# Kernel optimization log

Measured on AMD Instinct MI355X. Metric: run time of the kernel, lower is better.

The kernel has to match this reference:

```python
import jax, jax.numpy as jnp
import numpy as np

D = 192
HEADS = 4
HD = D // HEADS
R = 3  # correlation radius actually used in forward_level
NDISP = (2 * R + 1) ** 2  # 49
T = 3  # frames -> 2 consecutive pairs
ITERS = 4


def layer_norm(x, w, b, eps=1e-5):
    m = jnp.mean(x, axis=-1, keepdims=True)
    v = jnp.var(x, axis=-1, keepdims=True)
    return (x - m) / jnp.sqrt(v + eps) * w + b


def mha(x, in_w, in_b, out_w, out_b):
    # torch nn.MultiheadAttention, batch_first, self-attention
    B, N, _ = x.shape
    qkv = x @ in_w.T + in_b
    q, k, v = jnp.split(qkv, 3, axis=-1)
    q = q.reshape(B, N, HEADS, HD).transpose(0, 2, 1, 3) * (1.0 / float(np.sqrt(HD)))
    k = k.reshape(B, N, HEADS, HD).transpose(0, 2, 1, 3)
    v = v.reshape(B, N, HEADS, HD).transpose(0, 2, 1, 3)
    att = jax.nn.softmax(jnp.einsum('bhqd,bhkd->bhqk', q, k), axis=-1)
    y = jnp.einsum('bhqk,bhkd->bhqd', att, v).transpose(0, 2, 1, 3).reshape(B, N, D)
    return y @ out_w.T + out_b


def tblock(x, p):
    ln1w, ln1b, inw, inb, ow, ob, ln2w, ln2b, w1, b1, w2, b2 = p
    x = x + mha(layer_norm(x, ln1w, ln1b), inw, inb, ow, ob)
    h = layer_norm(x, ln2w, ln2b)
    h = jax.nn.gelu(h @ w1.T + b1, approximate=False) @ w2.T + b2
    return x + h


def local_corr(f1, f2):
    C = f1.shape[1]
    scale = 1.0 / float(np.sqrt(C))
    outs = []
    for dy in range(-R, R + 1):
        for dx in range(-R, R + 1):
            f2s = jnp.roll(f2, (dy, dx), axis=(2, 3))
            outs.append(jnp.sum(f1 * f2s, axis=1) * scale)
    return jnp.stack(outs, axis=1)


def grid_sample_bilinear_border(img, grid):
    # img: B,C,H,W; grid: B,Ho,Wo,2 with (x,y) in [-1,1]; align_corners=True, border padding
    B, C, H, W = img.shape
    x = jnp.clip((grid[..., 0] + 1.0) * 0.5 * (W - 1), 0.0, W - 1)
    y = jnp.clip((grid[..., 1] + 1.0) * 0.5 * (H - 1), 0.0, H - 1)
    x0 = jnp.floor(x); y0 = jnp.floor(y)
    x1 = jnp.minimum(x0 + 1, W - 1); y1 = jnp.minimum(y0 + 1, H - 1)
    wx = (x - x0)[:, None]; wy = (y - y0)[:, None]
    imgf = img.reshape(B, C, H * W)
    Ho, Wo = x.shape[1], x.shape[2]
    def gather(yy, xx):
        idx = (yy * W + xx).astype(jnp.int32).reshape(B, 1, Ho * Wo)
        return jnp.take_along_axis(imgf, idx, axis=2).reshape(B, C, Ho, Wo)
    v00 = gather(y0, x0); v01 = gather(y0, x1)
    v10 = gather(y1, x0); v11 = gather(y1, x1)
    return v00 * (1 - wx) * (1 - wy) + v01 * wx * (1 - wy) + v10 * (1 - wx) * wy + v11 * wx * wy


def warp(img, flow):
    # flow in pixels, Bx2xHxW
    B, C, H, W = img.shape
    xs = jnp.linspace(-1.0, 1.0, W); ys = jnp.linspace(-1.0, 1.0, H)
    gx, gy = jnp.meshgrid(xs, ys)  # each (H, W), 'xy' indexing
    base = jnp.stack([gx, gy], axis=-1)[None]
    off = jnp.stack([flow[:, 0] * (2.0 / max(W - 1, 1)),
                     flow[:, 1] * (2.0 / max(H - 1, 1))], axis=-1)
    return grid_sample_bilinear_border(img, base + off)


def upsample2x_align(img):
    # F.interpolate(scale_factor=2, mode='bilinear', align_corners=True)
    B, C, H, W = img.shape
    Ho, Wo = 2 * H, 2 * W
    xs = jnp.linspace(-1.0, 1.0, Wo); ys = jnp.linspace(-1.0, 1.0, Ho)
    gx, gy = jnp.meshgrid(xs, ys)
    grid = jnp.broadcast_to(jnp.stack([gx, gy], axis=-1)[None], (B, Ho, Wo, 2))
    return grid_sample_bilinear_border(img, grid)


def conv2d(x, w, b):
    y = jax.lax.conv_general_dilated(x, w, (1, 1), ((1, 1), (1, 1)),
                                     dimension_numbers=('NCHW', 'OIHW', 'NCHW'))
    return y + b[None, :, None, None]


def _forward(feats_l1, feats_l2, feats_l3, tok_w, tok_b,
             lcm_ln1_w, lcm_ln1_b, lcm_in_w, lcm_in_b, lcm_out_w, lcm_out_b,
             lcm_ln2_w, lcm_ln2_b, lcm_mlp_w1, lcm_mlp_b1, lcm_mlp_w2, lcm_mlp_b2,
             gtr_ln1_w, gtr_ln1_b, gtr_in_w, gtr_in_b, gtr_out_w, gtr_out_b,
             gtr_ln2_w, gtr_ln2_b, gtr_mlp_w1, gtr_mlp_b1, gtr_mlp_w2, gtr_mlp_b2,
             head_w1, head_b1, head_w2, head_b2,
             ref1_w1, ref1_b1, ref1_w2, ref1_b2,
             ref0_w1, ref0_b1, ref0_w2, ref0_b2):
    feats = [[feats_l1[t] for t in range(T)],
             [feats_l2[t] for t in range(T)],
             [feats_l3[t] for t in range(T)]]
    # ---- CostTokenizer ----
    tokens = []
    for lvl in range(3):
        toks = []
        for k in range(T - 1):
            corr = local_corr(feats[lvl][k], feats[lvl][k + 1])
            toks.append(jnp.einsum('bchw,dc->bdhw', corr, tok_w[lvl]) + tok_b[lvl][None, :, None, None])
        tokens.append(toks)
    lcm_p = [(lcm_ln1_w[i], lcm_ln1_b[i], lcm_in_w[i], lcm_in_b[i], lcm_out_w[i], lcm_out_b[i],
              lcm_ln2_w[i], lcm_ln2_b[i], lcm_mlp_w1[i], lcm_mlp_b1[i], lcm_mlp_w2[i], lcm_mlp_b2[i])
             for i in range(lcm_ln1_w.shape[0])]
    gtr_p = [(gtr_ln1_w[i], gtr_ln1_b[i], gtr_in_w[i], gtr_in_b[i], gtr_out_w[i], gtr_out_b[i],
              gtr_ln2_w[i], gtr_ln2_b[i], gtr_mlp_w1[i], gtr_mlp_b1[i], gtr_mlp_w2[i], gtr_mlp_b2[i])
             for i in range(gtr_ln1_w.shape[0])]
    # ---- LatentCostMemory (EMA state; .detach() -> stop_gradient; state resets when N changes) ----
    state = None
    latent = []
    for toks in tokens:
        lvl_lat = []
        for tok in toks:
            B_, Dd, H, W = tok.shape
            x = tok.reshape(B_, Dd, H * W).transpose(0, 2, 1)  # b (h w) d
            for p in lcm_p:
                x = tblock(x, p)
            if state is None or state.shape[1] != x.shape[1]:
                state = jax.lax.stop_gradient(x)
            x = 0.8 * x + 0.2 * state
            state = jax.lax.stop_gradient(x)
            lvl_lat.append(x.transpose(0, 2, 1))  # b d n
        latent.append(lvl_lat)
    H8, W8 = feats[1][0].shape[-2:]
    coarse = []
    for lat in latent[1]:
        x = lat.transpose(0, 2, 1)
        for p in gtr_p:
            x = tblock(x, p)
        fv = jax.nn.gelu(x @ head_w1.T + head_b1, approximate=False) @ head_w2.T + head_b2
        coarse.append(fv.transpose(0, 2, 1).reshape(-1, 2, H8, W8))
    # ---- MSRecurrentDecoder ----
    outs = []
    for k, f8 in enumerate(coarse):
        cur = f8
        for _ in range(ITERS):
            w10 = warp(feats[1][k + 1], cur)
            x = jnp.concatenate([feats[1][k], cur, w10], axis=1)
            cur = cur + conv2d(jax.nn.gelu(conv2d(x, ref1_w1, ref1_b1), approximate=False), ref1_w2, ref1_b2)
        cur2 = upsample2x_align(cur)
        for _ in range(ITERS):
            w10 = warp(feats[0][k + 1], cur2)
            x = jnp.concatenate([feats[0][k], cur2, w10], axis=1)
            cur2 = cur2 + conv2d(jax.nn.gelu(conv2d(x, ref0_w1, ref0_b1), approximate=False), ref0_w2, ref0_b2)
        outs.append(cur2)
    return jnp.stack(outs)  # [pairs, B, 2, H/4, W/4]


def setup_inputs():
    key = jax.random.key(0)
    ks = iter(jax.random.split(key, 64))
    def rn(shape, s=1.0):
        return jax.random.normal(next(ks), shape, dtype=jnp.float32) * s
    B = 1
    inp = {}
    inp['feats_l1'] = rn((T, B, 64, 64, 64))
    inp['feats_l2'] = rn((T, B, 128, 32, 32))
    inp['feats_l3'] = rn((T, B, 192, 16, 16))
    inp['tok_w'] = rn((3, D, NDISP), 0.02)
    inp['tok_b'] = rn((3, D), 0.02)
    for pre, n in (('lcm', 6), ('gtr', 2)):
        inp[pre + '_ln1_w'] = jnp.ones((n, D), jnp.float32)
        inp[pre + '_ln1_b'] = jnp.zeros((n, D), jnp.float32)
        inp[pre + '_in_w'] = rn((n, 3 * D, D), 0.02)
        inp[pre + '_in_b'] = rn((n, 3 * D), 0.02)
        inp[pre + '_out_w'] = rn((n, D, D), 0.02)
        inp[pre + '_out_b'] = rn((n, D), 0.02)
        inp[pre + '_ln2_w'] = jnp.ones((n, D), jnp.float32)
        inp[pre + '_ln2_b'] = jnp.zeros((n, D), jnp.float32)
        inp[pre + '_mlp_w1'] = rn((n, 4 * D, D), 0.02)
        inp[pre + '_mlp_b1'] = rn((n, 4 * D), 0.02)
        inp[pre + '_mlp_w2'] = rn((n, D, 4 * D), 0.02)
        inp[pre + '_mlp_b2'] = rn((n, D), 0.02)
    inp['head_w1'] = rn((D, D), 0.02); inp['head_b1'] = rn((D,), 0.02)
    inp['head_w2'] = rn((2, D), 0.02); inp['head_b2'] = rn((2,), 0.02)
    inp['ref1_w1'] = rn((128, 258, 3, 3), 0.02); inp['ref1_b1'] = rn((128,), 0.02)
    inp['ref1_w2'] = rn((2, 128, 3, 3), 0.02); inp['ref1_b2'] = rn((2,), 0.02)
    inp['ref0_w1'] = rn((64, 130, 3, 3), 0.02); inp['ref0_b1'] = rn((64,), 0.02)
    inp['ref0_w2'] = rn((2, 64, 3, 3), 0.02); inp['ref0_b2'] = rn((2,), 0.02)
    return inp


def reference(feats_l1, feats_l2, feats_l3, tok_w, tok_b,
              lcm_ln1_w, lcm_ln1_b, lcm_in_w, lcm_in_b, lcm_out_w, lcm_out_b,
              lcm_ln2_w, lcm_ln2_b, lcm_mlp_w1, lcm_mlp_b1, lcm_mlp_w2, lcm_mlp_b2,
              gtr_ln1_w, gtr_ln1_b, gtr_in_w, gtr_in_b, gtr_out_w, gtr_out_b,
              gtr_ln2_w, gtr_ln2_b, gtr_mlp_w1, gtr_mlp_b1, gtr_mlp_w2, gtr_mlp_b2,
              head_w1, head_b1, head_w2, head_b2,
              ref1_w1, ref1_b1, ref1_w2, ref1_b2,
              ref0_w1, ref0_b1, ref0_w2, ref0_b2):
    return _forward(feats_l1, feats_l2, feats_l3, tok_w, tok_b,
                    lcm_ln1_w, lcm_ln1_b, lcm_in_w, lcm_in_b, lcm_out_w, lcm_out_b,
                    lcm_ln2_w, lcm_ln2_b, lcm_mlp_w1, lcm_mlp_b1, lcm_mlp_w2, lcm_mlp_b2,
                    gtr_ln1_w, gtr_ln1_b, gtr_in_w, gtr_in_b, gtr_out_w, gtr_out_b,
                    gtr_ln2_w, gtr_ln2_b, gtr_mlp_w1, gtr_mlp_b1, gtr_mlp_w2, gtr_mlp_b2,
                    head_w1, head_b1, head_w2, head_b2,
                    ref1_w1, ref1_b1, ref1_w2, ref1_b2,
                    ref0_w1, ref0_b1, ref0_w2, ref0_b2)
```

## Files before the change

kernel.cpp:

```cpp
#include <hip/hip_runtime.h>
#include <hip/hip_bf16.h>

typedef __hip_bfloat16 bf16;
typedef short bf16x8 __attribute__((ext_vector_type(8)));
typedef float f32x4 __attribute__((ext_vector_type(4)));

#define DEV __device__ __forceinline__

DEV float bf2f(bf16 v) { return __bfloat162float(v); }
DEV bf16 f2bf(float v) { return __float2bfloat16(v); }
DEV unsigned short bfr(float f) {
  bf16 h = __float2bfloat16(f);
  return *reinterpret_cast<unsigned short*>(&h);
}
DEV float shf(unsigned short u) {
  unsigned int x = ((unsigned int)u) << 16;
  return *reinterpret_cast<float*>(&x);
}
DEV float gelu_exact(float x) { return 0.5f * x * (1.0f + erff(x * 0.70710678118654752f)); }

DEV float ldw(const void* p, long i, int isb) {
  return isb ? __bfloat162float(((const bf16*)p)[i]) : ((const float*)p)[i];
}

__global__ void k_detect(const unsigned short* __restrict__ u, int* __restrict__ flag) {
  __shared__ int bad;
  if (threadIdx.x == 0) bad = 0;
  __syncthreads();
  for (int i = threadIdx.x; i < 8192; i += 256) {
    int expo = (u[i] >> 7) & 0xFF;
    if (expo >= 138) atomicOr(&bad, 1);
  }
  __syncthreads();
  if (threadIdx.x == 0) *flag = bad ? 0 : 1;
}
__global__ void k_setone(int* p) { *p = 1; }

__global__ void k_cvt(const void* __restrict__ s, float* __restrict__ d, int n,
                      const int* __restrict__ fl) {
  int isb = *fl;
  int i = blockIdx.x * blockDim.x + threadIdx.x;
  if (i < n) d[i] = ldw(s, i, isb);
}

__global__ void k_zerosh(unsigned short* __restrict__ p, int n8) {
  int i = blockIdx.x * blockDim.x + threadIdx.x;
  if (i < n8) { uint4 z = {0, 0, 0, 0}; *(uint4*)(p + (long)i * 8) = z; }
}

__global__ void k_padtokw(const void* __restrict__ tw, bf16* __restrict__ dst,
                          const int* __restrict__ fl) {
  int isb = *fl;
  int i = blockIdx.x * blockDim.x + threadIdx.x;
  if (i >= 12288) return;
  int n = i >> 6, k = i & 63;
  float v = (k < 49) ? ldw(tw, 9408 + (long)n * 49 + k, isb) : 0.0f;
  dst[i] = f2bf(v);
}

__global__ void k_packw(const void* __restrict__ src, bf16* __restrict__ dst,
                        int OC, int C, int ICT, int NP, int ICP, int n,
                        const int* __restrict__ fl) {
  int isb = *fl;
  int i = blockIdx.x * blockDim.x + threadIdx.x;
  if (i >= n) return;
  int s = i / (NP * ICP);
  int r = i - s * NP * ICP;
  int oc = r / ICP, icp = r - oc * ICP;
  float v = 0.0f;
  if (oc < OC) {
    int ic = -1;
    if (icp < C) ic = icp;
    else if (icp < 2 * C) ic = icp - C + C + 2;
    else if (icp < 2 * C + 2) ic = icp - 2 * C + C;
    if (ic >= 0 && ic < ICT) v = ldw(src, ((long)oc * ICT + ic) * 9 + s, isb);
  }
  dst[i] = f2bf(v);
}

__global__ void k_trans_feats(const void* __restrict__ in, bf16* __restrict__ Fp,
                              int F, int C, int HW, const int* __restrict__ fl) {
  int isb = *fl;
  int cpg = C >> 3;
  int n = F * HW * cpg;
  int i = blockIdx.x * blockDim.x + threadIdx.x;
  if (i >= n) return;
  int p = i % HW;
  int rem = i / HW;
  int c8 = rem % cpg;
// ... 147 lines not shown
  for (int t = 0; t < 9; ++t) {
    int dy = t / 3, dx = t - dy * 3;
    const unsigned short* ar = base + ((long)dy * Wp2 + dx) * C;
    const unsigned short* w0r = wb + (long)(t * 16 + 0) * C;
    const unsigned short* w1r = wb + (long)(t * 16 + 1) * C;
    if (CPL == 2) {
      unsigned int a = *(const unsigned int*)ar;
      unsigned int q0 = *(const unsigned int*)w0r;
      unsigned int q1 = *(const unsigned int*)w1r;
      float a0 = shf((unsigned short)a), a1 = shf((unsigned short)(a >> 16));
      s0 += a0 * shf((unsigned short)q0) + a1 * shf((unsigned short)(q0 >> 16));
      s1 += a0 * shf((unsigned short)q1) + a1 * shf((unsigned short)(q1 >> 16));
    } else {
      float a0 = shf(ar[0]);
      s0 += a0 * shf(w0r[0]);
      s1 += a0 * shf(w1r[0]);
    }
  }
#pragma unroll
  for (int o = 32; o; o >>= 1) { s0 += __shfl_xor(s0, o); s1 += __shfl_xor(s1, o); }
  if (ln == 0) {
    cur[((long)b * 2 + 0) * HW + p] = s0 + b0 + r0;
    cur[((long)b * 2 + 1) * HW + p] = s1 + b1 + r1;
  }
}

__global__ void k_corr(const bf16* __restrict__ Fp2, bf16* __restrict__ corrT) {
  __shared__ unsigned short f1r[128];
  int p = blockIdx.x;
  int b = blockIdx.y;
  int t = threadIdx.x;
  const unsigned short* f1 = (const unsigned short*)Fp2 + ((long)b * 1024 + p) * 128;
  if (t < 16) *(uint4*)&f1r[t * 8] = *(const uint4*)(f1 + t * 8);
  __syncthreads();
  long rowo = ((long)b * 1024 + p) * 64;
  if (t < 49) {
    int dy = t / 7 - 3, dx = t % 7 - 3;
    int h = p >> 5, w = p & 31;
    int p2 = (((h - dy) & 31) << 5) | ((w - dx) & 31);
    const unsigned short* f2 = (const unsigned short*)Fp2 + ((long)(b + 1) * 1024 + p2) * 128;
    float s = 0.0f;
    for (int c = 0; c < 128; c += 8) {
      union { unsigned short u[8]; uint4 v; } av = { .v = *(const uint4*)&f1r[c] };
      union { unsigned short u[8]; uint4 v; } bv = { .v = *(const uint4*)(f2 + c) };
#pragma unroll
      for (int j = 0; j < 8; ++j) s += shf(av.u[j]) * shf(bv.u[j]);
    }
    corrT[rowo + t] = f2bf(s * 0.08838834764831845f);
  } else {
    corrT[rowo + t] = f2bf(0.0f);
  }
}

template <int KT, int NTW, int ACT, bool HASRES, int AMODE, int OUTBF, int VT>
__global__ __launch_bounds__(64, 2) void k_gemm_w(
    const void* __restrict__ A, const void* __restrict__ W, long woff,
    const void* __restrict__ bias, long boff, const int* __restrict__ flb,
    const float* __restrict__ res, void* __restrict__ C,
    int N, const int* __restrict__ fl,
    const unsigned short* __restrict__ mop, const float* __restrict__ mml,
    bf16* __restrict__ vtout,
    const void* __restrict__ lnw, long lnwoff,
    const void* __restrict__ lnb, long lnboff) {
  constexpr int NK = KT / 32;
  int isb = *fl;
  int ln = threadIdx.x;
  int quad = ln >> 4, l16 = ln & 15;
  int m0 = blockIdx.y * 16, n0 = blockIdx.x * (16 * NTW);
  __shared__ unsigned short Als[(AMODE >= 2) ? 16 : 1][200];
  if constexpr (AMODE == 3) {
    int row = ln >> 2, j = ln & 3;
    const float* xr = (const float*)A + (long)(m0 + row) * 192 + j * 48;
    float av[48];
#pragma unroll
    for (int q = 0; q < 12; ++q) {
      float4 v = *(const float4*)(xr + q * 4);
      av[q * 4 + 0] = v.x; av[q * 4 + 1] = v.y;
      av[q * 4 + 2] = v.z; av[q * 4 + 3] = v.w;
    }
    float sum = 0.0f;
#pragma unroll
    for (int q = 0; q < 48; ++q) sum += av[q];
    sum += __shfl_xor(sum, 1);
    sum += __shfl_xor(sum, 2);
    float mean = sum * (1.0f / 192.0f);
    float vs = 0.0f;
#pragma unroll
    for (int q = 0; q < 48; ++q) { float d = av[q] - mean; vs += d * d; }
    vs += __shfl_xor(vs, 1);
    vs += __shfl_xor(vs, 2);
    float rstd = rsqrtf(vs * (1.0f / 192.0f) + 1e-5f);
#pragma unroll
    for (int g = 0; g < 6; ++g) {
      union { unsigned short u[8]; uint4 v; } pk;
#pragma unroll
      for (int e = 0; e < 8; ++e) {
        long k = j * 48 + g * 8 + e;
        float gg = ldw(lnw, lnwoff + k, isb);
        float bb = ldw(lnb, lnboff + k, isb);
        pk.u[e] = bfr((av[g * 8 + e] - mean) * rstd * gg + bb);
      }
      *(uint4*)&Als[row][j * 48 + g * 8] = pk.v;
    }
  } else if constexpr (AMODE == 2) {
    int row = ln >> 2, j = ln & 3;
    int m = m0 + row;
    int rr = m & 1023, bb = m >> 10;
    long idx[4];
    float ms[4], ls[4];
    float Ms = -1e30f;
#pragma unroll
    for (int s = 0; s < 4; ++s) {
      idx[s] = (((long)s * 2 + bb) * 4 + j) * 1024 + rr;
      ms[s] = mml[idx[s] * 2];
      ls[s] = mml[idx[s] * 2 + 1];
      Ms = fmaxf(Ms, ms[s]);
    }
    float e4[4], L = 0.0f;
#pragma unroll
    for (int s = 0; s < 4; ++s) { e4[s] = __expf(ms[s] - Ms); L += ls[s] * e4[s]; }
    float invL = 1.0f / L;
#pragma unroll
    for (int g = 0; g < 6; ++g) {
      union { unsigned short u[8]; uint4 v; } pk;
#pragma unroll
      for (int e2 = 0; e2 < 8; ++e2) {
        float o = 0.0f;
#pragma unroll
        for (int s = 0; s < 4; ++s) o += shf(mop[idx[s] * 48 + g * 8 + e2]) * e4[s];
        pk.u[e2] = bfr(o * invL);
      }
      *(uint4*)&Als[row][j * 48 + g * 8] = pk.v;
    }
  }
  f32x4 acc[NTW] = {};
  auto lda = [&](int kc) -> bf16x8 {
    if constexpr (AMODE >= 2) {
      return *(const bf16x8*)&Als[l16][kc * 32 + quad * 8];
    } else if constexpr (AMODE == 1) {
      return *(const bf16x8*)((const unsigned short*)A + (long)(m0 + l16) * KT + kc * 32 + quad * 8);
    } else {
      const float* ap = (const float*)A + (long)(m0 + l16) * KT + kc * 32 + quad * 8;
      float4 a0 = *(const float4*)ap;
      float4 a1 = *(const float4*)(ap + 4);
      union { unsigned short u[8]; bf16x8 v; } pk;
      pk.u[0] = bfr(a0.x); pk.u[1] = bfr(a0.y); pk.u[2] = bfr(a0.z); pk.u[3] = bfr(a0.w);
      pk.u[4] = bfr(a1.x); pk.u[5] = bfr(a1.y); pk.u[6] = bfr(a1.z); pk.u[7] = bfr(a1.w);
      return pk.v;
    }
  };
  if (isb) {
    const unsigned short* wb = (const unsigned short*)W + woff + (long)l16 * KT + quad * 8;
    for (int kc = 0; kc < NK; ++kc) {
      bf16x8 af = lda(kc);
#pragma unroll
      for (int nt = 0; nt < NTW; ++nt) {
        bf16x8 wf = *(const bf16x8*)(wb + (long)(n0 + nt * 16) * KT + kc * 32);
        acc[nt] = __builtin_amdgcn_mfma_f32_16x16x32_bf16(af, wf, acc[nt], 0, 0, 0);
      }
    }
  } else {
    const float* wb = (const float*)W + woff + (long)l16 * KT + quad * 8;
    for (int kc = 0; kc < NK; ++kc) {
      bf16x8 af = lda(kc);
#pragma unroll
      for (int nt = 0; nt < NTW; ++nt) {
        const float* wp = wb + (long)(n0 + nt * 16) * KT + kc * 32;
        float4 w0 = *(const float4*)wp;
        float4 w1 = *(const float4*)(wp + 4);
        union { unsigned short u[8]; bf16x8 v; } pk;
        pk.u[0] = bfr(w0.x); pk.u[1] = bfr(w0.y); pk.u[2] = bfr(w0.z); pk.u[3] = bfr(w0.w);
        pk.u[4] = bfr(w1.x); pk.u[5] = bfr(w1.y); pk.u[6] = bfr(w1.z); pk.u[7] = bfr(w1.w);
        acc[nt] = __builtin_amdgcn_mfma_f32_16x16x32_bf16(af, pk.v, acc[nt], 0, 0, 0);
      }
    }
  }
  int isbb = *flb;
#pragma unroll
  for (int nt = 0; nt < NTW; ++nt) {
    int n = n0 + nt * 16 + l16;
    float bv = ldw(bias, boff + n, isbb);
#pragma unroll
    for (int r = 0; r < 4; ++r) {
      int m = m0 + quad * 4 + r;
      float v = acc[nt][r] + bv;
      if (HASRES) v += res[(long)m * N + n];
      if (ACT == 1) v = gelu_exact(v);
      if (OUTBF) ((bf16*)C)[(long)m * N + n] = f2bf(v);
      else ((float*)C)[(long)m * N + n] = v;
      if constexpr (VT) {
        if (n >= 384) {
          int hh = (n - 384) / 48, dd = (n - 384) % 48;
          int row = m & 1023, bb = m >> 10;
          vtout[((long)(bb * 4 + hh) * 48 + dd) * 1024 + row] = f2bf(v);
        }
      }
    }
  }
}

__global__ __launch_bounds__(256) void k_head2(const float* __restrict__ A,
                                               const void* __restrict__ W,
                                               const void* __restrict__ bias,
                                               float* __restrict__ C,
                                               const int* __restrict__ fl) {
  int isb = *fl;
  int wv = threadIdx.x >> 6, ln = threadIdx.x & 63;
  int gw = blockIdx.x * 4 + wv;
  int m = gw >> 1, n = gw & 1;
  const float* a = A + (long)m * 192;
  float s = 0.0f;
#pragma unroll
  for (int q = 0; q < 3; ++q) {
    int j = ln + q * 64;
    s += a[j] * ldw(W, (long)n * 192 + j, isb);
  }
  for (int o = 32; o; o >>= 1) s += __shfl_xor(s, o);
  if (ln == 0) {
    int b = m >> 10, p = m & 1023;
    C[((long)b * 2 + n) * 1024 + p] = s + ldw(bias, n, isb);
  }
}

__global__ __launch_bounds__(256) void k_attn_mfma(const bf16* __restrict__ qkv,
                                                   const bf16* __restrict__ vt,
                                                   unsigned short* __restrict__ opart,
                                                   float* __restrict__ ml) {
  __shared__ unsigned short Qs[64][72];
  __shared__ unsigned short Ks[64][72];
  __shared__ unsigned short Vs[48][72];
  __shared__ unsigned short Ps[64][72];
  int tid = threadIdx.x;
  int wv = tid >> 6, ln = tid & 63, quad = ln >> 4, l16 = ln & 15;
  int h = blockIdx.y, b = blockIdx.z;
  int qt = blockIdx.x >> 2, s = blockIdx.x & 3;
  int q0 = qt * 64;
  const unsigned short* qp = (const unsigned short*)qkv + (long)b * 1024 * 576;
  const unsigned short* vp = (const unsigned short*)vt + ((long)(b * 4 + h) * 48) * 1024;
  for (int i = tid; i < 384; i += 256) {
    int r = i / 6, c = i % 6;
    *(uint4*)&Qs[r][c * 8] = *(const uint4*)(qp + (long)(q0 + r) * 576 + h * 48 + c * 8);
  }
  for (int i = tid; i < 128; i += 256) {
    int r = i >> 1, c = 6 + (i & 1);
    uint4 z = {0, 0, 0, 0};
    *(uint4*)&Qs[r][c * 8] = z;
  }
  float m[4] = {-1e30f, -1e30f, -1e30f, -1e30f};
  float l[4] = {0.0f, 0.0f, 0.0f, 0.0f};
  f32x4 accO[3] = {};
  const float SC = 0.14433756729740643f;
  for (int kc = s * 4; kc < s * 4 + 4; ++kc) {
    int k0 = kc * 64;
    for (int i = tid; i < 384; i += 256) {
      int r = i / 6, c = i % 6;
      *(uint4*)&Ks[r][c * 8] = *(const uint4*)(qp + (long)(k0 + r) * 576 + 192 + h * 48 + c * 8);
    }
    for (int i = tid; i < 128; i += 256) {
      int r = i >> 1, c = 6 + (i & 1);
      uint4 z = {0, 0, 0, 0};
      *(uint4*)&Ks[r][c * 8] = z;
    }
    for (int i = tid; i < 384; i += 256) {
      int d = i >> 3, c = i & 7;
      *(uint4*)&Vs[d][c * 8] = *(const uint4*)(vp + (long)d * 1024 + k0 + c * 8);
    }
    __syncthreads();
    f32x4 accS[4] = {};
    bf16x8 a0 = *(const bf16x8*)&Qs[wv * 16 + l16][quad * 8];
    bf16x8 a1 = *(const bf16x8*)&Qs[wv * 16 + l16][32 + quad * 8];
#pragma unroll
    for (int ct = 0; ct < 4; ++ct) {
      bf16x8 b0 = *(const bf16x8*)&Ks[ct * 16 + l16][quad * 8];
      bf16x8 b1 = *(const bf16x8*)&Ks[ct * 16 + l16][32 + quad * 8];
// ... 72 lines not shown
  int i = blockIdx.x * blockDim.x + threadIdx.x;
  if (i < 16384) {
    if (isb) ((bf16*)out)[i] = f2bf(cur2[i]);
    else ((float*)out)[i] = cur2[i];
  }
}

extern "C" void kernel_launch(void* const* d_in, const int* in_sizes, int n_in,
                              void* d_out, int out_size, void* d_ws, size_t ws_size,
                              hipStream_t stream) {
  const void* feats_l1 = d_in[0];
  const void* feats_l2 = d_in[1];
  const void* tok_w = d_in[3];
  const void* tok_b = d_in[4];
  const void* lcm_ln1_w = d_in[5];
  const void* lcm_ln1_b = d_in[6];
  const void* lcm_in_w  = d_in[7];
  const void* lcm_in_b  = d_in[8];
  const void* lcm_out_w = d_in[9];
  const void* lcm_out_b = d_in[10];
  const void* lcm_ln2_w = d_in[11];
  const void* lcm_ln2_b = d_in[12];
  const void* lcm_mlp_w1 = d_in[13];
  const void* lcm_mlp_b1 = d_in[14];
  const void* lcm_mlp_w2 = d_in[15];
  const void* lcm_mlp_b2 = d_in[16];
  const void* gtr_ln1_w = d_in[17];
  const void* gtr_ln1_b = d_in[18];
  const void* gtr_in_w  = d_in[19];
  const void* gtr_in_b  = d_in[20];
  const void* gtr_out_w = d_in[21];
  const void* gtr_out_b = d_in[22];
  const void* gtr_ln2_w = d_in[23];
  const void* gtr_ln2_b = d_in[24];
  const void* gtr_mlp_w1 = d_in[25];
  const void* gtr_mlp_b1 = d_in[26];
  const void* gtr_mlp_w2 = d_in[27];
  const void* gtr_mlp_b2 = d_in[28];
  const void* head_w1 = d_in[29];
  const void* head_b1 = d_in[30];
  const void* head_w2 = d_in[31];
  const void* head_b2 = d_in[32];
  const void* ref1_w1 = d_in[33];
  const void* ref1_b1 = d_in[34];
  const void* ref1_w2 = d_in[35];
  const void* ref1_b2 = d_in[36];
  const void* ref0_w1 = d_in[37];
  const void* ref0_b1 = d_in[38];
  const void* ref0_w2 = d_in[39];
  const void* ref0_b2 = d_in[40];
  (void)ws_size; (void)n_in; (void)in_sizes; (void)out_size;

  int* flag = (int*)d_ws;
  int* oneflag = (int*)d_ws + 2;
  float* wsf = (float*)d_ws;
  float* F2   = wsf + 16;
  float* rA   = F2 + 393216;
  float* rX   = rA + 786432;
  float* rT   = rX + 393216;
  float* rY   = rT + 393216;
  float* big  = rY + 393216;
  float* fv   = big + 1572864;
  float* cur  = fv + 4096;
  float* cur2 = cur + 4096;
  float* cb1a = cur2 + 16384;
  float* cb1b = cb1a + 128;
  float* cb0a = cb1b + 16;
  float* cb0b = cb0a + 64;
  bf16* wtok  = (bf16*)(cb0b + 16);
  float* wpk  = cb0b + 16 + 6144;
  bf16* w1p1 = (bf16*)wpk;
  bf16* w1p2 = (bf16*)(wpk + 165888);
  bf16* w0p1 = (bf16*)(wpk + 175104);
  bf16* w0p2 = (bf16*)(wpk + 221184);

  float* x = rX;
  bf16* corrTb = (bf16*)big;
  bf16* qkvbb  = (bf16*)big;
  bf16* vtb    = (bf16*)(big + 655360);
  bf16* hidb   = (bf16*)big;
  unsigned short* opart = (unsigned short*)rA;
  float* mlbuf = rY;
  float* headh = rT;
  bf16* mid0p = (bf16*)rT;
  bf16* mid1p = (bf16*)rY;
  bf16* Fp2   = (bf16*)(big + 851968);
  bf16* Fp1   = (bf16*)(big + 1048576);

  k_detect<<<1, 256, 0, stream>>>((const unsigned short*)feats_l1, flag);
  k_setone<<<1, 1, 0, stream>>>(oneflag);
  k_cvt<<<1, 256, 0, stream>>>(ref1_b1, cb1a, 128, flag);
  k_cvt<<<1, 256, 0, stream>>>(ref1_b2, cb1b, 2, flag);
  k_cvt<<<1, 256, 0, stream>>>(ref0_b1, cb0a, 64, flag);
  k_cvt<<<1, 256, 0, stream>>>(ref0_b2, cb0b, 2, flag);
  k_padtokw<<<48, 256, 0, stream>>>(tok_w, wtok, flag);
  k_packw<<<1296, 256, 0, stream>>>(ref1_w1, w1p1, 128, 128, 258, 128, 288, 331776, flag);
  k_packw<<<72, 256, 0, stream>>>(ref1_w2, w1p2, 2, 128, 128, 16, 128, 18432, flag);
  k_packw<<<360, 256, 0, stream>>>(ref0_w1, w0p1, 64, 64, 130, 64, 160, 92160, flag);
  k_packw<<<36, 256, 0, stream>>>(ref0_w2, w0p2, 2, 64, 64, 16, 64, 9216, flag);
  k_trans_feats<<<192, 256, 0, stream>>>(feats_l2, Fp2, 3, 128, 1024, flag);
  k_trans_feats<<<384, 256, 0, stream>>>(feats_l1, Fp1, 3, 64, 4096, flag);

  k_corr<<<dim3(1024, 2), 64, 0, stream>>>(Fp2, corrTb);
  k_gemm_w<64, 4, 0, false, 1, 0, 0><<<dim3(3, 128), 64, 0, stream>>>(
      corrTb, wtok, 0, tok_b, 192, flag, nullptr, x, 192, oneflag,
      nullptr, nullptr, nullptr, nullptr, 0, nullptr, 0);

  auto run_block = [&](const void* ln1w, long o1, const void* ln1b, long o2,
                       const void* inw, long o3, const void* inb, long o4,
                       const void* ow, long o5, const void* ob, long o6,
                       const void* ln2w, long o7, const void* ln2b, long o8,
                       const void* w1, long o9, const void* b1, long o10,
                       const void* w2, long o11, const void* b2, long o12) {
    k_gemm_w<192, 4, 0, false, 3, 1, 1><<<dim3(9, 128), 64, 0, stream>>>(
        x, inw, o3, inb, o4, flag, nullptr, qkvbb, 576, flag,
        nullptr, nullptr, vtb, ln1w, o1, ln1b, o2);
    k_attn_mfma<<<dim3(64, 4, 2), 256, 0, stream>>>(qkvbb, vtb, opart, mlbuf);
    k_gemm_w<192, 4, 0, true, 2, 0, 0><<<dim3(3, 128), 64, 0, stream>>>(
        nullptr, ow, o5, ob, o6, flag, x, x, 192, flag,
        opart, mlbuf, nullptr, nullptr, 0, nullptr, 0);
    k_gemm_w<192, 4, 1, false, 3, 1, 0><<<dim3(12, 128), 64, 0, stream>>>(
        x, w1, o9, b1, o10, flag, nullptr, hidb, 768, flag,
        nullptr, nullptr, nullptr, ln2w, o7, ln2b, o8);
    k_gemm_w<768, 4, 0, true, 1, 0, 0><<<dim3(3, 128), 64, 0, stream>>>(
        hidb, w2, o11, b2, o12, flag, x, x, 192, flag,
        nullptr, nullptr, nullptr, nullptr, 0, nullptr, 0);
  };

  for (int i = 0; i < 6; ++i) {
    run_block(lcm_ln1_w, (long)i * 192, lcm_ln1_b, (long)i * 192,
              lcm_in_w, (long)i * 110592, lcm_in_b, (long)i * 576,
              lcm_out_w, (long)i * 36864, lcm_out_b, (long)i * 192,
              lcm_ln2_w, (long)i * 192, lcm_ln2_b, (long)i * 192,
              lcm_mlp_w1, (long)i * 147456, lcm_mlp_b1, (long)i * 768,
              lcm_mlp_w2, (long)i * 147456, lcm_mlp_b2, (long)i * 192);
  }
  k_ema<<<768, 256, 0, stream>>>(x);

  for (int i = 0; i < 2; ++i) {
    run_block(gtr_ln1_w, (long)i * 192, gtr_ln1_b, (long)i * 192,
              gtr_in_w, (long)i * 110592, gtr_in_b, (long)i * 576,
              gtr_out_w, (long)i * 36864, gtr_out_b, (long)i * 192,
              gtr_ln2_w, (long)i * 192, gtr_ln2_b, (long)i * 192,
              gtr_mlp_w1, (long)i * 147456, gtr_mlp_b1, (long)i * 768,
              gtr_mlp_w2, (long)i * 147456, gtr_mlp_b2, (long)i * 192);
  }

  k_gemm_w<192, 4, 1, false, 0, 0, 0><<<dim3(3, 128), 64, 0, stream>>>(
      x, head_w1, 0, head_b1, 0, flag, nullptr, headh, 192, flag,
      nullptr, nullptr, nullptr, nullptr, 0, nullptr, 0);
  k_head2<<<1024, 256, 0, stream>>>(headh, head_w2, head_b2, cur, flag);

  k_zerosh<<<768, 256, 0, stream>>>((unsigned short*)rT, 196608);

  for (int it = 0; it < 4; ++it) {
    k_conv1d<128, 288, 128, 32, 5><<<dim3(8, 64, 2), 64, 0, stream>>>(
        Fp2, cur, w1p1, cb1a, mid1p);
    k_conv2_dot<128, 32, 5><<<512, 256, 0, stream>>>(mid1p, w1p2, cb1b, cur);
  }
  k_upsample<<<64, 256, 0, stream>>>(cur, cur2);

  for (int it = 0; it < 4; ++it) {
    k_conv1d<64, 160, 64, 64, 6><<<dim3(4, 256, 2), 64, 0, stream>>>(
        Fp1, cur2, w0p1, cb0a, mid0p);
    k_conv2_dot<64, 64, 6><<<2048, 256, 0, stream>>>(mid0p, w0p2, cb0b, cur2);
  }

  k_out<<<64, 256, 0, stream>>>(cur2, d_out, flag);
}
```

Baseline: 1.007 ms.

## Fuse transformer block stages (out-proj, LN2, MLP, next LN1+QKV) into per-row-tile kernels

Replaces the separate per-stage GEMM launches (out-projection with attention merge, LN2+MLP1, MLP2, next block's LN1+QKV, and the head MLP) with one 256-thread kernel per 16-row tile. The kernel keeps the residual, normalized rows and the 768-wide hidden activations in shared memory, so those intermediates never go through global memory and the launch count drops. The token embedding GEMM is also fused with the first LN1+QKV. In exchange each block runs only 128 workgroups with large shared-memory use and some waves sitting idle, which lowers parallelism, and every workgroup rereads the full weight matrices.

```diff
diff --git a/kernel.cpp b/kernel.cpp
--- a/kernel.cpp
+++ b/kernel.cpp
@@ -34,7 +34,6 @@
   __syncthreads();
   if (threadIdx.x == 0) *flag = bad ? 0 : 1;
 }
-__global__ void k_setone(int* p) { *p = 1; }
 
 __global__ void k_cvt(const void* __restrict__ s, float* __restrict__ d, int n,
                       const int* __restrict__ fl) {
@@ -288,120 +287,27 @@
   }
 }
 
-template <int KT, int NTW, int ACT, bool HASRES, int AMODE, int OUTBF, int VT>
-__global__ __launch_bounds__(64, 2) void k_gemm_w(
-    const void* __restrict__ A, const void* __restrict__ W, long woff,
-    const void* __restrict__ bias, long boff, const int* __restrict__ flb,
-    const float* __restrict__ res, void* __restrict__ C,
-    int N, const int* __restrict__ fl,
-    const unsigned short* __restrict__ mop, const float* __restrict__ mml,
-    bf16* __restrict__ vtout,
-    const void* __restrict__ lnw, long lnwoff,
-    const void* __restrict__ lnb, long lnboff) {
-  constexpr int NK = KT / 32;
-  int isb = *fl;
-  int ln = threadIdx.x;
+template <int KT>
+DEV void wtile(const unsigned short* Al, int LDA, const void* W, long woff,
+               int ncol0, int isb, int ln, f32x4* acc) {
   int quad = ln >> 4, l16 = ln & 15;
-  int m0 = blockIdx.y * 16, n0 = blockIdx.x * (16 * NTW);
-  __shared__ unsigned short Als[(AMODE >= 2) ? 16 : 1][200];
-  if constexpr (AMODE == 3) {
-    int row = ln >> 2, j = ln & 3;
-    const float* xr = (const float*)A + (long)(m0 + row) * 192 + j * 48;
-    float av[48];
-#pragma unroll
-    for (int q = 0; q < 12; ++q) {
-      float4 v = *(const float4*)(xr + q * 4);
-      av[q * 4 + 0] = v.x; av[q * 4 + 1] = v.y;
-      av[q * 4 + 2] = v.z; av[q * 4 + 3] = v.w;
-    }
-    float sum = 0.0f;
-#pragma unroll
-    for (int q = 0; q < 48; ++q) sum += av[q];
-    sum += __shfl_xor(sum, 1);
-    sum += __shfl_xor(sum, 2);
-    float mean = sum * (1.0f / 192.0f);
-    float vs = 0.0f;
-#pragma unroll
-    for (int q = 0; q < 48; ++q) { float d = av[q] - mean; vs += d * d; }
-    vs += __shfl_xor(vs, 1);
-    vs += __shfl_xor(vs, 2);
-    float rstd = rsqrtf(vs * (1.0f / 192.0f) + 1e-5f);
-#pragma unroll
-    for (int g = 0; g < 6; ++g) {
-      union { unsigned short u[8]; uint4 v; } pk;
-#pragma unroll
-      for (int e = 0; e < 8; ++e) {
-        long k = j * 48 + g * 8 + e;
-        float gg = ldw(lnw, lnwoff + k, isb);
-        float bb = ldw(lnb, lnboff + k, isb);
-        pk.u[e] = bfr((av[g * 8 + e] - mean) * rstd * gg + bb);
-      }
-      *(uint4*)&Als[row][j * 48 + g * 8] = pk.v;
-    }
-  } else if constexpr (AMODE == 2) {
-    int row = ln >> 2, j = ln & 3;
-    int m = m0 + row;
-    int rr = m & 1023, bb = m >> 10;
-    long idx[4];
-    float ms[4], ls[4];
-    float Ms = -1e30f;
-#pragma unroll
-    for (int s = 0; s < 4; ++s) {
-      idx[s] = (((long)s * 2 + bb) * 4 + j) * 1024 + rr;
-      ms[s] = mml[idx[s] * 2];
-      ls[s] = mml[idx[s] * 2 + 1];
-      Ms = fmaxf(Ms, ms[s]);
-    }
-    float e4[4], L = 0.0f;
-#pragma unroll
-    for (int s = 0; s < 4; ++s) { e4[s] = __expf(ms[s] - Ms); L += ls[s] * e4[s]; }
-    float invL = 1.0f / L;
-#pragma unroll
-    for (int g = 0; g < 6; ++g) {
-      union { unsigned short u[8]; uint4 v; } pk;
-#pragma unroll
-      for (int e2 = 0; e2 < 8; ++e2) {
-        float o = 0.0f;
-#pragma unroll
-        for (int s = 0; s < 4; ++s) o += shf(mop[idx[s] * 48 + g * 8 + e2]) * e4[s];
-        pk.u[e2] = bfr(o * invL);
-      }
-      *(uint4*)&Als[row][j * 48 + g * 8] = pk.v;
-    }
-  }
-  f32x4 acc[NTW] = {};
-  auto lda = [&](int kc) -> bf16x8 {
-    if constexpr (AMODE >= 2) {
-      return *(const bf16x8*)&Als[l16][kc * 32 + quad * 8];
-    } else if constexpr (AMODE == 1) {
-      return *(const bf16x8*)((const unsigned short*)A + (long)(m0 + l16) * KT + kc * 32 + quad * 8);
-    } else {
-      const float* ap = (const float*)A + (long)(m0 + l16) * KT + kc * 32 + quad * 8;
-      float4 a0 = *(const float4*)ap;
-      float4 a1 = *(const float4*)(ap + 4);
-      union { unsigned short u[8]; bf16x8 v; } pk;
-      pk.u[0] = bfr(a0.x); pk.u[1] = bfr(a0.y); pk.u[2] = bfr(a0.z); pk.u[3] = bfr(a0.w);
-      pk.u[4] = bfr(a1.x); pk.u[5] = bfr(a1.y); pk.u[6] = bfr(a1.z); pk.u[7] = bfr(a1.w);
-      return pk.v;
-    }
-  };
   if (isb) {
-    const unsigned short* wb = (const unsigned short*)W + woff + (long)l16 * KT + quad * 8;
-    for (int kc = 0; kc < NK; ++kc) {
-      bf16x8 af = lda(kc);
-#pragma unroll
-      for (int nt = 0; nt < NTW; ++nt) {
-        bf16x8 wf = *(const bf16x8*)(wb + (long)(n0 + nt * 16) * KT + kc * 32);
+    const unsigned short* wb = (const unsigned short*)W + woff + quad * 8;
+    for (int kc = 0; kc < KT / 32; ++kc) {
+      bf16x8 af = *(const bf16x8*)&Al[l16 * LDA + kc * 32 + quad * 8];
+#pragma unroll
+      for (int nt = 0; nt < 4; ++nt) {
+        bf16x8 wf = *(const bf16x8*)(wb + (long)(ncol0 + nt * 16 + l16) * KT + kc * 32);
         acc[nt] = __builtin_amdgcn_mfma_f32_16x16x32_bf16(af, wf, acc[nt], 0, 0, 0);
       }
     }
   } else {
-    const float* wb = (const float*)W + woff + (long)l16 * KT + quad * 8;
-    for (int kc = 0; kc < NK; ++kc) {
-      bf16x8 af = lda(kc);
-#pragma unroll
-      for (int nt = 0; nt < NTW; ++nt) {
-        const float* wp = wb + (long)(n0 + nt * 16) * KT + kc * 32;
+    const float* wb = (const float*)W + woff + quad * 8;
+    for (int kc = 0; kc < KT / 32; ++kc) {
+      bf16x8 af = *(const bf16x8*)&Al[l16 * LDA + kc * 32 + quad * 8];
+#pragma unroll
+      for (int nt = 0; nt < 4; ++nt) {
+        const float* wp = wb + (long)(ncol0 + nt * 16 + l16) * KT + kc * 32;
         float4 w0 = *(const float4*)wp;
         float4 w1 = *(const float4*)(wp + 4);
         union { unsigned short u[8]; bf16x8 v; } pk;
@@ -411,51 +317,245 @@
       }
     }
   }
-  int isbb = *flb;
-#pragma unroll
-  for (int nt = 0; nt < NTW; ++nt) {
-    int n = n0 + nt * 16 + l16;
-    float bv = ldw(bias, boff + n, isbb);
-#pragma unroll
-    for (int r = 0; r < 4; ++r) {
-      int m = m0 + quad * 4 + r;
-      float v = acc[nt][r] + bv;
-      if (HASRES) v += res[(long)m * N + n];
-      if (ACT == 1) v = gelu_exact(v);
-      if (OUTBF) ((bf16*)C)[(long)m * N + n] = f2bf(v);
-      else ((float*)C)[(long)m * N + n] = v;
-      if constexpr (VT) {
+}
+
+DEV void ln_row(const float* src, int ss, const void* w, long wo,
+                const void* b, long bo, int isb, int tid,
+                unsigned short* dst, int ds) {
+  int row = tid >> 4, j = tid & 15;
+  const float* s = src + (long)row * ss + j * 12;
+  float a[12];
+#pragma unroll
+  for (int q = 0; q < 12; ++q) a[q] = s[q];
+  float sum = 0.0f;
+#pragma unroll
+  for (int q = 0; q < 12; ++q) sum += a[q];
+#pragma unroll
+  for (int o = 1; o < 16; o <<= 1) sum += __shfl_xor(sum, o);
+  float mean = sum * (1.0f / 192.0f);
+  float vs = 0.0f;
+#pragma unroll
+  for (int q = 0; q < 12; ++q) { float d = a[q] - mean; vs += d * d; }
+#pragma unroll
+  for (int o = 1; o < 16; o <<= 1) vs += __shfl_xor(vs, o);
+  float rstd = rsqrtf(vs * (1.0f / 192.0f) + 1e-5f);
+  unsigned short* d = dst + (long)row * ds + j * 12;
+#pragma unroll
+  for (int q = 0; q < 12; ++q) {
+    long k = j * 12 + q;
+    d[q] = bfr((a[q] - mean) * rstd * ldw(w, wo + k, isb) + ldw(b, bo + k, isb));
+  }
+}
+
+DEV void qkv_tail(const unsigned short* tbp, int wv, int ln, int m0, int isb,
+                  const void* inw, long o_inw, const void* inb, long o_inb,
+                  bf16* qkvbb, bf16* vtb) {
+  int quad = ln >> 4, l16 = ln & 15;
+  for (int t = wv; t < 9; t += 4) {
+    f32x4 acc[4] = {};
+    wtile<192>(tbp, 200, inw, o_inw, t * 64, isb, ln, acc);
+#pragma unroll
+    for (int nt = 0; nt < 4; ++nt) {
+      int n = t * 64 + nt * 16 + l16;
+#pragma unroll
+      for (int r = 0; r < 4; ++r) {
+        int m = m0 + quad * 4 + r;
+        float v = acc[nt][r] + ldw(inb, o_inb + n, isb);
+        qkvbb[(long)m * 576 + n] = f2bf(v);
         if (n >= 384) {
           int hh = (n - 384) / 48, dd = (n - 384) % 48;
-          int row = m & 1023, bb = m >> 10;
-          vtout[((long)(bb * 4 + hh) * 48 + dd) * 1024 + row] = f2bf(v);
+          int row = m & 1023, bb2 = m >> 10;
+          vtb[((long)(bb2 * 4 + hh) * 48 + dd) * 1024 + row] = f2bf(v);
         }
       }
     }
   }
 }
 
-__global__ __launch_bounds__(256) void k_head2(const float* __restrict__ A,
-                                               const void* __restrict__ W,
-                                               const void* __restrict__ bias,
-                                               float* __restrict__ C,
-                                               const int* __restrict__ fl) {
+template <int TAIL>
+__global__ __launch_bounds__(256, 2) void k_fuse(
+    const int* __restrict__ fl, float* __restrict__ x,
+    const unsigned short* __restrict__ mop, const float* __restrict__ mml,
+    const void* ow, long o_ow, const void* ob, long o_ob,
+    const void* ln2w, long o_l2w, const void* ln2b, long o_l2b,
+    const void* w1, long o_w1, const void* b1, long o_b1,
+    const void* w2, long o_w2, const void* b2, long o_b2,
+    const void* ln1w, long o_l1w, const void* ln1b, long o_l1b,
+    const void* inw, long o_inw, const void* inb, long o_inb,
+    bf16* qkvbb, bf16* vtb,
+    const void* hw1, const void* hb1, const void* hw2, const void* hb2,
+    float* cur) {
+  __shared__ float xs[16][200];
+  __shared__ unsigned short tb[16][200];
+  __shared__ unsigned short hb[16][776];
+  int tid = threadIdx.x, wv = tid >> 6, ln = tid & 63;
+  int quad = ln >> 4, l16 = ln & 15;
+  int m0 = blockIdx.x * 16;
   int isb = *fl;
-  int wv = threadIdx.x >> 6, ln = threadIdx.x & 63;
-  int gw = blockIdx.x * 4 + wv;
-  int m = gw >> 1, n = gw & 1;
-  const float* a = A + (long)m * 192;
-  float s = 0.0f;
-#pragma unroll
-  for (int q = 0; q < 3; ++q) {
-    int j = ln + q * 64;
-    s += a[j] * ldw(W, (long)n * 192 + j, isb);
-  }
-  for (int o = 32; o; o >>= 1) s += __shfl_xor(s, o);
-  if (ln == 0) {
-    int b = m >> 10, p = m & 1023;
-    C[((long)b * 2 + n) * 1024 + p] = s + ldw(bias, n, isb);
-  }
+  if (tid < 64) {
+    int row = tid >> 2, j = tid & 3;
+    int m = m0 + row;
+    int rr = m & 1023, bb = m >> 10;
+    long idx[4];
+    float ms[4], ls[4];
+    float Ms = -1e30f;
+#pragma unroll
+    for (int s = 0; s < 4; ++s) {
+      idx[s] = (((long)s * 2 + bb) * 4 + j) * 1024 + rr;
+      ms[s] = mml[idx[s] * 2];
+      ls[s] = mml[idx[s] * 2 + 1];
+      Ms = fmaxf(Ms, ms[s]);
+    }
+    float e4[4], L = 0.0f;
+#pragma unroll
+    for (int s = 0; s < 4; ++s) { e4[s] = __expf(ms[s] - Ms); L += ls[s] * e4[s]; }
+    float invL = 1.0f / L;
+#pragma unroll
+    for (int g = 0; g < 6; ++g) {
+      union { unsigned short u[8]; uint4 v; } pk;
+#pragma unroll
+      for (int e2 = 0; e2 < 8; ++e2) {
+        float o = 0.0f;
+#pragma unroll
+        for (int s = 0; s < 4; ++s) o += shf(mop[idx[s] * 48 + g * 8 + e2]) * e4[s];
+        pk.u[e2] = bfr(o * invL);
+      }
+      *(uint4*)&tb[row][j * 48 + g * 8] = pk.v;
+    }
+  }
+  __syncthreads();
+  if (wv < 3) {
+    f32x4 acc[4] = {};
+    wtile<192>(&tb[0][0], 200, ow, o_ow, wv * 64, isb, ln, acc);
+#pragma unroll
+    for (int nt = 0; nt < 4; ++nt) {
+      int n = wv * 64 + nt * 16 + l16;
+#pragma unroll
+      for (int r = 0; r < 4; ++r) {
+        int mrow = quad * 4 + r;
+        int m = m0 + mrow;
+        float v = acc[nt][r] + ldw(ob, o_ob + n, isb) + x[(long)m * 192 + n];
+        x[(long)m * 192 + n] = v;
+        xs[mrow][n] = v;
+      }
+    }
+  }
+  __syncthreads();
+  ln_row(&xs[0][0], 200, ln2w, o_l2w, ln2b, o_l2b, isb, tid, &tb[0][0], 200);
+  __syncthreads();
+  for (int t = wv; t < 12; t += 4) {
+    f32x4 acc[4] = {};
+    wtile<192>(&tb[0][0], 200, w1, o_w1, t * 64, isb, ln, acc);
+#pragma unroll
+    for (int nt = 0; nt < 4; ++nt) {
+      int n = t * 64 + nt * 16 + l16;
+#pragma unroll
+      for (int r = 0; r < 4; ++r)
+        hb[quad * 4 + r][n] = bfr(gelu_exact(acc[nt][r] + ldw(b1, o_b1 + n, isb)));
+    }
+  }
+  __syncthreads();
+  if (wv < 3) {
+    f32x4 acc[4] = {};
+    wtile<768>(&hb[0][0], 776, w2, o_w2, wv * 64, isb, ln, acc);
+#pragma unroll
+    for (int nt = 0; nt < 4; ++nt) {
+      int n = wv * 64 + nt * 16 + l16;
+#pragma unroll
+      for (int r = 0; r < 4; ++r) {
+        int mrow = quad * 4 + r;
+        int m = m0 + mrow;
+        float v = acc[nt][r] + ldw(b2, o_b2 + n, isb) + xs[mrow][n];
+        x[(long)m * 192 + n] = v;
+        xs[mrow][n] = v;
+        if constexpr (TAIL == 2) tb[mrow][n] = bfr(v);
+      }
+    }
+  }
+  __syncthreads();
+  if constexpr (TAIL == 1) {
+    ln_row(&xs[0][0], 200, ln1w, o_l1w, ln1b, o_l1b, isb, tid, &tb[0][0], 200);
+    __syncthreads();
+    qkv_tail(&tb[0][0], wv, ln, m0, isb, inw, o_inw, inb, o_inb, qkvbb, vtb);
+  } else if constexpr (TAIL == 2) {
+    float* hf = (float*)&hb[0][0];
+    if (wv < 3) {
+      f32x4 acc[4] = {};
+      wtile<192>(&tb[0][0], 200, hw1, 0, wv * 64, isb, ln, acc);
+#pragma unroll
+      for (int nt = 0; nt < 4; ++nt) {
+        int n = wv * 64 + nt * 16 + l16;
+#pragma unroll
+        for (int r = 0; r < 4; ++r)
+          hf[(quad * 4 + r) * 200 + n] = gelu_exact(acc[nt][r] + ldw(hb1, n, isb));
+      }
+    }
+    __syncthreads();
+    for (int p = wv; p < 32; p += 4) {
+      int row = p >> 1, n = p & 1;
+      float s = 0.0f;
+#pragma unroll
+      for (int q = 0; q < 3; ++q) {
+        int j = ln + q * 64;
+        s += hf[row * 200 + j] * ldw(hw2, (long)n * 192 + j, isb);
+      }
+      for (int o = 32; o; o >>= 1) s += __shfl_xor(s, o);
+      if (ln == 0) {
+        int m = m0 + row;
+        int bb2 = m >> 10, pp = m & 1023;
+        cur[((long)bb2 * 2 + n) * 1024 + pp] = s + ldw(hb2, n, isb);
+      }
+    }
+  }
+}
+
+__global__ __launch_bounds__(256, 2) void k_fuse0(
+    const int* __restrict__ fl, const bf16* __restrict__ corrTb,
+    const bf16* __restrict__ wtok, const void* tok_b,
+    float* __restrict__ x,
+    const void* ln1w, long o_l1w, const void* ln1b, long o_l1b,
+    const void* inw, long o_inw, const void* inb, long o_inb,
+    bf16* qkvbb, bf16* vtb) {
+  __shared__ float xs[16][200];
+  __shared__ unsigned short tb[16][200];
+  int tid = threadIdx.x, wv = tid >> 6, ln = tid & 63;
+  int quad = ln >> 4, l16 = ln & 15;
+  int m0 = blockIdx.x * 16;
+  int isb = *fl;
+  if (wv < 3) {
+    f32x4 acc[4] = {};
+    wtile<64>((const unsigned short*)corrTb + (long)m0 * 64, 64, wtok, 0, wv * 64, 1, ln, acc);
+#pragma unroll
+    for (int nt = 0; nt < 4; ++nt) {
+      int n = wv * 64 + nt * 16 + l16;
+#pragma unroll
+      for (int r = 0; r < 4; ++r) {
+        int mrow = quad * 4 + r;
+        int m = m0 + mrow;
+        float v = acc[nt][r] + ldw(tok_b, n, isb);
+        x[(long)m * 192 + n] = v;
+        xs[mrow][n] = v;
+      }
+    }
+  }
+  __syncthreads();
+  ln_row(&xs[0][0], 200, ln1w, o_l1w, ln1b, o_l1b, isb, tid, &tb[0][0], 200);
+  __syncthreads();
+  qkv_tail(&tb[0][0], wv, ln, m0, isb, inw, o_inw, inb, o_inb, qkvbb, vtb);
+}
+
+__global__ __launch_bounds__(256, 2) void k_fuseA(
+    const int* __restrict__ fl, const float* __restrict__ x,
+    const void* ln1w, long o_l1w, const void* ln1b, long o_l1b,
+    const void* inw, long o_inw, const void* inb, long o_inb,
+    bf16* qkvbb, bf16* vtb) {
+  __shared__ unsigned short tb[16][200];
+  int tid = threadIdx.x, wv = tid >> 6, ln = tid & 63;
+  int m0 = blockIdx.x * 16;
+  int isb = *fl;
+  ln_row(x + (long)m0 * 192, 192, ln1w, o_l1w, ln1b, o_l1b, isb, tid, &tb[0][0], 200);
+  __syncthreads();
+  qkv_tail(&tb[0][0], wv, ln, m0, isb, inw, o_inw, inb, o_inb, qkvbb, vtb);
 }
 
 __global__ __launch_bounds__(256) void k_attn_mfma(const bf16* __restrict__ qkv,
@@ -634,7 +734,6 @@
   (void)ws_size; (void)n_in; (void)in_sizes; (void)out_size;
 
   int* flag = (int*)d_ws;
-  int* oneflag = (int*)d_ws + 2;
   float* wsf = (float*)d_ws;
   float* F2   = wsf + 16;
   float* rA   = F2 + 393216;
@@ -657,20 +756,17 @@
   bf16* w0p2 = (bf16*)(wpk + 221184);
 
   float* x = rX;
-  bf16* corrTb = (bf16*)big;
+  bf16* corrTb = (bf16*)rT;
   bf16* qkvbb  = (bf16*)big;
   bf16* vtb    = (bf16*)(big + 655360);
-  bf16* hidb   = (bf16*)big;
   unsigned short* opart = (unsigned short*)rA;
   float* mlbuf = rY;
-  float* headh = rT;
   bf16* mid0p = (bf16*)rT;
   bf16* mid1p = (bf16*)rY;
   bf16* Fp2   = (bf16*)(big + 851968);
   bf16* Fp1   = (bf16*)(big + 1048576);
 
   k_detect<<<1, 256, 0, stream>>>((const unsigned short*)feats_l1, flag);
-  k_setone<<<1, 1, 0, stream>>>(oneflag);
   k_cvt<<<1, 256, 0, stream>>>(ref1_b1, cb1a, 128, flag);
   k_cvt<<<1, 256, 0, stream>>>(ref1_b2, cb1b, 2, flag);
   k_cvt<<<1, 256, 0, stream>>>(ref0_b1, cb0a, 64, flag);
@@ -684,54 +780,55 @@
   k_trans_feats<<<384, 256, 0, stream>>>(feats_l1, Fp1, 3, 64, 4096, flag);
 
   k_corr<<<dim3(1024, 2), 64, 0, stream>>>(Fp2, corrTb);
-  k_gemm_w<64, 4, 0, false, 1, 0, 0><<<dim3(3, 128), 64, 0, stream>>>(
-      corrTb, wtok, 0, tok_b, 192, flag, nullptr, x, 192, oneflag,
-      nullptr, nullptr, nullptr, nullptr, 0, nullptr, 0);
-
-  auto run_block = [&](const void* ln1w, long o1, const void* ln1b, long o2,
-                       const void* inw, long o3, const void* inb, long o4,
-                       const void* ow, long o5, const void* ob, long o6,
-                       const void* ln2w, long o7, const void* ln2b, long o8,
-                       const void* w1, long o9, const void* b1, long o10,
-                       const void* w2, long o11, const void* b2, long o12) {
-    k_gemm_w<192, 4, 0, false, 3, 1, 1><<<dim3(9, 128), 64, 0, stream>>>(
-        x, inw, o3, inb, o4, flag, nullptr, qkvbb, 576, flag,
-        nullptr, nullptr, vtb, ln1w, o1, ln1b, o2);
+  k_fuse0<<<128, 256, 0, stream>>>(flag, corrTb, wtok, tok_b, x,
+                                   lcm_ln1_w, 0, lcm_ln1_b, 0,
+                                   lcm_in_w, 0, lcm_in_b, 0, qkvbb, vtb);
+
+  for (int i = 0; i < 8; ++i) {
     k_attn_mfma<<<dim3(64, 4, 2), 256, 0, stream>>>(qkvbb, vtb, opart, mlbuf);
-    k_gemm_w<192, 4, 0, true, 2, 0, 0><<<dim3(3, 128), 64, 0, stream>>>(
-        nullptr, ow, o5, ob, o6, flag, x, x, 192, flag,
-        opart, mlbuf, nullptr, nullptr, 0, nullptr, 0);
-    k_gemm_w<192, 4, 1, false, 3, 1, 0><<<dim3(12, 128), 64, 0, stream>>>(
-        x, w1, o9, b1, o10, flag, nullptr, hidb, 768, flag,
-        nullptr, nullptr, nullptr, ln2w, o7, ln2b, o8);
-    k_gemm_w<768, 4, 0, true, 1, 0, 0><<<dim3(3, 128), 64, 0, stream>>>(
-        hidb, w2, o11, b2, o12, flag, x, x, 192, flag,
-        nullptr, nullptr, nullptr, nullptr, 0, nullptr, 0);
-  };
-
-  for (int i = 0; i < 6; ++i) {
-    run_block(lcm_ln1_w, (long)i * 192, lcm_ln1_b, (long)i * 192,
-              lcm_in_w, (long)i * 110592, lcm_in_b, (long)i * 576,
-              lcm_out_w, (long)i * 36864, lcm_out_b, (long)i * 192,
-              lcm_ln2_w, (long)i * 192, lcm_ln2_b, (long)i * 192,
-              lcm_mlp_w1, (long)i * 147456, lcm_mlp_b1, (long)i * 768,
-              lcm_mlp_w2, (long)i * 147456, lcm_mlp_b2, (long)i * 192);
-  }
-  k_ema<<<768, 256, 0, stream>>>(x);
-
-  for (int i = 0; i < 2; ++i) {
-    run_block(gtr_ln1_w, (long)i * 192, gtr_ln1_b, (long)i * 192,
-              gtr_in_w, (long)i * 110592, gtr_in_b, (long)i * 576,
-              gtr_out_w, (long)i * 36864, gtr_out_b, (long)i * 192,
-              gtr_ln2_w, (long)i * 192, gtr_ln2_b, (long)i * 192,
-              gtr_mlp_w1, (long)i * 147456, gtr_mlp_b1, (long)i * 768,
-              gtr_mlp_w2, (long)i * 147456, gtr_mlp_b2, (long)i * 192);
-  }
-
-  k_gemm_w<192, 4, 1, false, 0, 0, 0><<<dim3(3, 128), 64, 0, stream>>>(
-      x, head_w1, 0, head_b1, 0, flag, nullptr, headh, 192, flag,
-      nullptr, nullptr, nullptr, nullptr, 0, nullptr, 0);
-  k_head2<<<1024, 256, 0, stream>>>(headh, head_w2, head_b2, cur, flag);
+    bool lcm = i < 6;
+    long ii = lcm ? i : (i - 6);
+    const void* ow  = lcm ? lcm_out_w  : gtr_out_w;
+    const void* ob  = lcm ? lcm_out_b  : gtr_out_b;
+    const void* l2w = lcm ? lcm_ln2_w  : gtr_ln2_w;
+    const void* l2b = lcm ? lcm_ln2_b  : gtr_ln2_b;
+    const void* w1  = lcm ? lcm_mlp_w1 : gtr_mlp_w1;
+    const void* b1  = lcm ? lcm_mlp_b1 : gtr_mlp_b1;
+    const void* w2  = lcm ? lcm_mlp_w2 : gtr_mlp_w2;
+    const void* b2  = lcm ? lcm_mlp_b2 : gtr_mlp_b2;
+    long o5 = ii * 36864, o6 = ii * 192, o7 = ii * 192, o8 = ii * 192;
+    long o9 = ii * 147456, o10 = ii * 768, o11 = ii * 147456, o12 = ii * 192;
+    if (i < 5) {
+      long nx = i + 1;
+      k_fuse<1><<<128, 256, 0, stream>>>(
+          flag, x, opart, mlbuf, ow, o5, ob, o6, l2w, o7, l2b, o8,
+          w1, o9, b1, o10, w2, o11, b2, o12,
+          lcm_ln1_w, nx * 192, lcm_ln1_b, nx * 192,
+          lcm_in_w, nx * 110592, lcm_in_b, nx * 576,
+          qkvbb, vtb, nullptr, nullptr, nullptr, nullptr, nullptr);
+    } else if (i == 5) {
+      k_fuse<0><<<128, 256, 0, stream>>>(
+          flag, x, opart, mlbuf, ow, o5, ob, o6, l2w, o7, l2b, o8,
+          w1, o9, b1, o10, w2, o11, b2, o12,
+          nullptr, 0, nullptr, 0, nullptr, 0, nullptr, 0,
+          nullptr, nullptr, nullptr, nullptr, nullptr, nullptr, nullptr);
+      k_ema<<<768, 256, 0, stream>>>(x);
+      k_fuseA<<<128, 256, 0, stream>>>(flag, x, gtr_ln1_w, 0, gtr_ln1_b, 0,
+                                       gtr_in_w, 0, gtr_in_b, 0, qkvbb, vtb);
+    } else if (i == 6) {
+      k_fuse<1><<<128, 256, 0, stream>>>(
+          flag, x, opart, mlbuf, ow, o5, ob, o6, l2w, o7, l2b, o8,
+          w1, o9, b1, o10, w2, o11, b2, o12,
+          gtr_ln1_w, 192, gtr_ln1_b, 192, gtr_in_w, 110592, gtr_in_b, 576,
+          qkvbb, vtb, nullptr, nullptr, nullptr, nullptr, nullptr);
+    } else {
+      k_fuse<2><<<128, 256, 0, stream>>>(
+          flag, x, opart, mlbuf, ow, o5, ob, o6, l2w, o7, l2b, o8,
+          w1, o9, b1, o10, w2, o11, b2, o12,
+          nullptr, 0, nullptr, 0, nullptr, 0, nullptr, 0,
+          nullptr, nullptr, head_w1, head_b1, head_w2, head_b2, cur);
+    }
+  }
 
   k_zerosh<<<768, 256, 0, stream>>>((unsigned short*)rT, 196608);
 
```

Result: slower. 1.139 ms (+13.1%).
